# Kernel tuning notes

Measured on AMD Instinct MI355X. Metric: run time of the kernel, lower is better.

## Reference

```python
import jax, jax.numpy as jnp
import numpy as np
from jax.ops import segment_sum, segment_max

NUM_USERS = 100000
NUM_ITEMS = 50000
N_TOTAL = NUM_USERS + NUM_ITEMS
D = 64
E = 2000000
GCN_LAYERS = 3
GCN_LEFT = 0.5
GCN_RIGHT = 0.5
GCN_MEAN = True
USE_CL = True
CL_EPS = 0.2
CL_LAYER = 1
RF_LAYERS = 2
RF_TAU = 0.5
RF_ALPHA = 1.0


def setup_inputs() -> dict:
    key = jax.random.key(0)
    k1, k2, k3, k4, k5 = jax.random.split(key, 5)
    return {
        "user_emb": 0.1 * jax.random.normal(k1, (NUM_USERS, D), dtype=jnp.float32),
        "item_emb": 0.1 * jax.random.normal(k2, (NUM_ITEMS, D), dtype=jnp.float32),
        "noise": jax.random.uniform(k3, (GCN_LAYERS, N_TOTAL, D), dtype=jnp.float32),
        "edge_u": jax.random.randint(k4, (E,), 0, NUM_USERS, dtype=jnp.int32),
        "edge_i": jax.random.randint(k5, (E,), 0, NUM_ITEMS, dtype=jnp.int32),
    }


def _gcn_layer(emb, edge_u, edge_i, cu, ci):
    # LightGCN-style degree-normalized bipartite propagation over the edge list.
    ue, ie = emb[:NUM_USERS], emb[NUM_USERS:]
    # messages item -> user and user -> item, normalized by deg^-left * deg^-right
    msg_u = segment_sum(ie[edge_i] * (cu[edge_u] * ci[edge_i])[:, None], edge_u,
                        num_segments=NUM_USERS)
    msg_i = segment_sum(ue[edge_u] * (ci[edge_i] * cu[edge_u])[:, None], edge_i,
                        num_segments=NUM_ITEMS)
    return jnp.concatenate([msg_u, msg_i], axis=0)


def _rankformer_layer(emb, edge_u, edge_i):
    # Edge-sparse attention: per-edge score, segment softmax per node, weighted aggregate.
    ue, ie = emb[:NUM_USERS], emb[NUM_USERS:]
    eu_g, ei_g = ue[edge_u], ie[edge_i]            # [E, D] gathers
    s = RF_ALPHA * jnp.sum(eu_g * ei_g, axis=-1)   # [E]
    # user-side softmax over incident items
    mu = segment_max(s, edge_u, num_segments=NUM_USERS)
    pu = jnp.exp(s - mu[edge_u])
    zu = segment_sum(pu, edge_u, num_segments=NUM_USERS)
    rec_u = segment_sum(pu[:, None] * ei_g, edge_u, num_segments=NUM_USERS)
    rec_u = rec_u / jnp.maximum(zu, 1e-9)[:, None]
    # item-side softmax over incident users
    mi = segment_max(s, edge_i, num_segments=NUM_ITEMS)
    pi = jnp.exp(s - mi[edge_i])
    zi = segment_sum(pi, edge_i, num_segments=NUM_ITEMS)
    rec_i = segment_sum(pi[:, None] * eu_g, edge_i, num_segments=NUM_ITEMS)
    rec_i = rec_i / jnp.maximum(zi, 1e-9)[:, None]
    return jnp.concatenate([rec_u, rec_i], axis=0)


def reference(user_emb, item_emb, noise, edge_u, edge_i):
    ones = jnp.ones((E,), dtype=user_emb.dtype)
    du = jnp.maximum(segment_sum(ones, edge_u, num_segments=NUM_USERS), 1.0)
    di = jnp.maximum(segment_sum(ones, edge_i, num_segments=NUM_ITEMS), 1.0)
    cu = du ** (-GCN_LEFT)   # user-side normalization (left exponent)
    ci = di ** (-GCN_RIGHT)  # item-side normalization (right exponent)

    emb = jnp.concatenate([user_emb, item_emb], axis=0)  # [N_TOTAL, D]
    layer_embs = [emb]
    for layer in range(GCN_LAYERS):
        emb = _gcn_layer(emb, edge_u, edge_i, cu, ci)
        if USE_CL:
            nz = noise[layer]
            nz = nz / jnp.maximum(jnp.linalg.norm(nz, axis=-1, keepdims=True), 1e-12)
            emb = emb + jnp.sign(emb) * nz * CL_EPS
        layer_embs.append(emb)
    if GCN_MEAN:
        emb = jnp.mean(jnp.stack(layer_embs, axis=-1), axis=-1)

    for _ in range(RF_LAYERS):
        rec = _rankformer_layer(emb, edge_u, edge_i)
        emb = (1.0 - RF_TAU) * emb + RF_TAU * rec
    return emb
```

## Files before the change

### kernel.cpp

```cpp
#include <hip/hip_runtime.h>
#include <math.h>

#pragma clang fp contract(off)
#pragma clang fp reassociate(off)

#define NU 100000
#define NI 50000
#define NT 150000
#define DD 64
#define NE 2000000
#define NTD (NT * DD)
#define NPART 8
#define PARTW_U (NU / NPART)
#define PARTW_I (NI / NPART)
#define NCHUNK 256
#define CHW ((NE + NCHUNK - 1) / NCHUNK)

typedef _Float16 half4 __attribute__((ext_vector_type(4)));

__global__ __launch_bounds__(256) void count_ui_k(const int* __restrict__ eu, const int* __restrict__ ei,
                                                  int* __restrict__ cnt) {
  int part = blockIdx.x & 7;
  int side = (blockIdx.x >> 3) & 1;
  int chunk = blockIdx.x >> 4;
  int e0 = chunk * CHW;
  int e1 = e0 + CHW; if (e1 > NE) e1 = NE;
  if (side == 0) {
    int lo = part * PARTW_U, hi = lo + PARTW_U;
    for (int e = e0 + threadIdx.x; e < e1; e += 256) {
      int u = eu[e];
      if (u >= lo && u < hi) atomicAdd(&cnt[u], 1);
    }
  } else {
    int lo = part * PARTW_I, hi = lo + PARTW_I;
    for (int e = e0 + threadIdx.x; e < e1; e += 256) {
      int it = ei[e];
      if (it >= lo && it < hi) atomicAdd(&cnt[NU + it], 1);
    }
  }
}

__global__ __launch_bounds__(1024) void scanA_k(const int* __restrict__ cnt, int* __restrict__ lexcl,
                                                int* __restrict__ partials, int n) {
  int idx = blockIdx.x * 1024 + threadIdx.x;
  int v = (idx < n) ? cnt[idx] : 0;
  int lane = threadIdx.x & 63;
  int wid = threadIdx.x >> 6;
  int x = v;
#pragma unroll
  for (int off = 1; off < 64; off <<= 1) {
    int y = __shfl_up(x, off, 64);
    if (lane >= off) x += y;
  }
  __shared__ int wtot[16], woff[16];
  if (lane == 63) wtot[wid] = x;
  __syncthreads();
  if (threadIdx.x == 0) {
    int a = 0;
#pragma unroll
    for (int w = 0; w < 16; ++w) { woff[w] = a; a += wtot[w]; }
    partials[blockIdx.x] = a;
  }
  __syncthreads();
  if (idx < n) lexcl[idx] = x - v + woff[wid];
}

__global__ __launch_bounds__(64) void scanB_k(int* __restrict__ partials, int* __restrict__ row, int nchunks) {
  int lane = threadIdx.x;
  int carry = 0;
  for (int base = 0; base < nchunks; base += 64) {
    int idx = base + lane;
    int v = (idx < nchunks) ? partials[idx] : 0;
    int x = v;
#pragma unroll
    for (int off = 1; off < 64; off <<= 1) {
      int y = __shfl_up(x, off, 64);
      if (lane >= off) x += y;
    }
    if (idx < nchunks) partials[idx] = carry + x - v;
    carry += __shfl(x, 63, 64);
  }
  if (lane == 0) row[NT] = carry;
}

__global__ __launch_bounds__(1024) void scanC_k(int* __restrict__ row, int* __restrict__ cursor,
                                                float* __restrict__ coef, const int* __restrict__ partials, int n) {
  int idx = blockIdx.x * 1024 + threadIdx.x;
  if (idx >= n) return;
  int c = cursor[idx];
  int fin = row[idx] + partials[blockIdx.x];
  row[idx] = fin;
  cursor[idx] = fin;
  coef[idx] = (float)pow((double)(c > 0 ? c : 1), -0.5);
}

__global__ __launch_bounds__(256) void fill_ui_k(const int* __restrict__ eu, const int* __restrict__ ei,
                                                 int* __restrict__ cursor, int* __restrict__ eid) {
  int part = blockIdx.x & 7;
  int side = (blockIdx.x >> 3) & 1;
  int chunk = blockIdx.x >> 4;
  int e0 = chunk * CHW;
  int e1 = e0 + CHW; if (e1 > NE) e1 = NE;
  if (side == 0) {
    int lo = part * PARTW_U, hi = lo + PARTW_U;
    for (int e = e0 + threadIdx.x; e < e1; e += 256) {
      int u = eu[e];
      if (u >= lo && u < hi) {
        int p = atomicAdd(&cursor[u], 1);
        eid[p] = e;
      }
    }
  } else {
    int lo = part * PARTW_I, hi = lo + PARTW_I;
    for (int e = e0 + threadIdx.x; e < e1; e += 256) {
      int it = ei[e];
      if (it >= lo && it < hi) {
        int p = atomicAdd(&cursor[NU + it], 1);
        eid[p] = e;
      }
    }
  }
}

__global__ __launch_bounds__(256) void sort_k(const int* __restrict__ row, const int* __restrict__ eid,
                                              const int* __restrict__ eu, const int* __restrict__ ei,
                                              int* __restrict__ col) {
  int wv = (blockIdx.x * blockDim.x + threadIdx.x) >> 6;
  int lane = threadIdx.x & 63;
  if (wv >= NT) return;
  int beg = row[wv], end = row[wv + 1];
  for (int idx = beg + lane; idx < end; idx += 64) {
    int my = eid[idx];
    int r = 0;
    for (int j = beg; j < end; ++j) r += (eid[j] < my);
    col[beg + r] = (wv < NU) ? (NU + ei[my]) : eu[my];
  }
}

template <int FIRST, int LAST>
__global__ __launch_bounds__(256) void gcn4_k(const float* __restrict__ in, float* __restrict__ out,
                                              float* __restrict__ acc,
                                              const int* __restrict__ row, const int* __restrict__ col,
                                              const float* __restrict__ coef, const float* __restrict__ nz_l,
                                              const float* __restrict__ ue, const float* __restrict__ ie,
                                              _Float16* __restrict__ h16out) {
  int wave = (blockIdx.x * blockDim.x + threadIdx.x) >> 6;
  int lane = threadIdx.x & 63;
  int g = lane >> 4, q = lane & 15;
  int node = wave * 4 + g;
  if (node >= NT) return;
  int beg = row[node], end = row[node + 1];
  float cn = coef[node];
  float sx = 0.f, sy = 0.f, sz = 0.f, sw = 0.f;

  const float* gbase;
  if (FIRST) {
    gbase = (node < NU) ? (ie - (size_t)NU * DD) : ue;
  } else {
    gbase = in;
  }

#define GLD(dv, dc, kk) { int m_ = col[kk]; dc = coef[m_]; dv = *(const float4*)(gbase + (size_t)m_ * DD + q * 4); }
  float4 cv0, cv1, cv2, cv3;
  float cc0, cc1, cc2, cc3;
  int rem = end - beg;
  int k4end = end - (rem & 3);
  int k = beg;
  if (k < k4end) {
    GLD(cv0, cc0, k) GLD(cv1, cc1, k + 1) GLD(cv2, cc2, k + 2) GLD(cv3, cc3, k + 3)
  }
  for (; k < k4end; k += 4) {
    float4 nv0, nv1, nv2, nv3;
    float nc0, nc1, nc2, nc3;
    bool more = (k + 4) < k4end;
    if (more) {
      GLD(nv0, nc0, k + 4) GLD(nv1, nc1, k + 5) GLD(nv2, nc2, k + 6) GLD(nv3, nc3, k + 7)
    }
    {
      float w = cn * cc0;
      sx = sx + (cv0.x * w); sy = sy + (cv0.y * w); sz = sz + (cv0.z * w); sw = sw + (cv0.w * w);
    }
    {
      float w = cn * cc1;
      sx = sx + (cv1.x * w); sy = sy + (cv1.y * w); sz = sz + (cv1.z * w); sw = sw + (cv1.w * w);
    }
    {
      float w = cn * cc2;
      sx = sx + (cv2.x * w); sy = sy + (cv2.y * w); sz = sz + (cv2.z * w); sw = sw + (cv2.w * w);
    }
    {
      float w = cn * cc3;
      sx = sx + (cv3.x * w); sy = sy + (cv3.y * w); sz = sz + (cv3.z * w); sw = sw + (cv3.w * w);
    }
    if (more) {
      cv0 = nv0; cc0 = nc0; cv1 = nv1; cc1 = nc1;
      cv2 = nv2; cc2 = nc2; cv3 = nv3; cc3 = nc3;
    }
  }
  for (; k < end; ++k) {
    float4 v; float c;
    GLD(v, c, k)
    float w = cn * c;
    sx = sx + (v.x * w); sy = sy + (v.y * w); sz = sz + (v.z * w); sw = sw + (v.w * w);
  }
#undef GLD

  float4 nzv = *(const float4*)(nz_l + (size_t)node * DD + q * 4);
  float4 sq;
  sq.x = nzv.x * nzv.x; sq.y = nzv.y * nzv.y;
  sq.z = nzv.z * nzv.z; sq.w = nzv.w * nzv.w;
  float rA0 = 0.f, rA1 = 0.f, rA2 = 0.f, rA3 = 0.f;
  float rB0 = 0.f, rB1 = 0.f, rB2 = 0.f, rB3 = 0.f;
  int base = g * 16;
#pragma unroll
  for (int kk = 0; kk < 8; ++kk) {
    int le = base + 2 * kk, lo = le + 1;
    rA0 = rA0 + __shfl(sq.x, le, 64);
    rA1 = rA1 + __shfl(sq.y, le, 64);
    rA2 = rA2 + __shfl(sq.z, le, 64);
    rA3 = rA3 + __shfl(sq.w, le, 64);
    rB0 = rB0 + __shfl(sq.x, lo, 64);
    rB1 = rB1 + __shfl(sq.y, lo, 64);
    rB2 = rB2 + __shfl(sq.z, lo, 64);
    rB3 = rB3 + __shfl(sq.w, lo, 64);
  }
  float t01 = rA0 + rA1, t23 = rA2 + rA3;
  float t45 = rB0 + rB1, t67 = rB2 + rB3;
  float tot = (t01 + t23) + (t45 + t67);
  float nrm = __fsqrt_rn(tot);
  float den = fmaxf(nrm, 1e-12f);
  float4 o;
  {
    float nn = nzv.x / den;
    float sg = (sx > 0.f) ? 1.f : ((sx < 0.f) ? -1.f : 0.f);
    o.x = sx + ((sg * nn) * 0.2f);
  }
  {
    float nn = nzv.y / den;
    float sg = (sy > 0.f) ? 1.f : ((sy < 0.f) ? -1.f : 0.f);
    o.y = sy + ((sg * nn) * 0.2f);
  }
  {
    float nn = nzv.z / den;
    float sg = (sz > 0.f) ? 1.f : ((sz < 0.f) ? -1.f : 0.f);
    o.z = sz + ((sg * nn) * 0.2f);
  }
  {
    float nn = nzv.w / den;
    float sg = (sw > 0.f) ? 1.f : ((sw < 0.f) ? -1.f : 0.f);
    o.w = sw + ((sg * nn) * 0.2f);
  }
  size_t boff = (size_t)node * DD + q * 4;
  if (FIRST) {
    const float* ownp = (node < NU) ? (ue + (size_t)node * DD) : (ie + (size_t)(node - NU) * DD);
    float4 own = *(const float4*)(ownp + q * 4);
    *(float4*)(out + boff) = o;
    float4 a;
    a.x = own.x + o.x; a.y = own.y + o.y; a.z = own.z + o.z; a.w = own.w + o.w;
    *(float4*)(acc + boff) = a;
  } else {
    float4 a = *(const float4*)(acc + boff);
    if (LAST) {
      float4 mo;
      mo.x = (a.x + o.x) * 0.25f;
      mo.y = (a.y + o.y) * 0.25f;
      mo.z = (a.z + o.z) * 0.25f;
      mo.w = (a.w + o.w) * 0.25f;
      *(float4*)(out + boff) = mo;
      half4 hh;
      hh.x = (_Float16)mo.x; hh.y = (_Float16)mo.y;
      hh.z = (_Float16)mo.z; hh.w = (_Float16)mo.w;
      *(half4*)(h16out + boff) = hh;
    } else {
      *(float4*)(out + boff) = o;
      a.x = a.x + o.x; a.y = a.y + o.y; a.z = a.z + o.z; a.w = a.w + o.w;
      *(float4*)(acc + boff) = a;
    }
  }
}

template <int WRITEH>
__global__ __launch_bounds__(256) void rfaccum_k(const float* __restrict__ inF,
                                                 const _Float16* __restrict__ inH,
                                                 float* __restrict__ outF,
                                                 _Float16* __restrict__ outH,
                                                 const int* __restrict__ row, const int* __restrict__ col) {
  int wave = (blockIdx.x * blockDim.x + threadIdx.x) >> 6;
  int lane = threadIdx.x & 63;
  int g = lane >> 4, q = lane & 15;
  int node = wave * 4 + g;
  if (node >= NT) return;
  int beg = row[node], end = row[node + 1];
  size_t boff = (size_t)node * DD + q * 4;
  float4 e = *(const float4*)(inF + boff);
  float rx = 0.f, ry = 0.f, rz = 0.f, rw = 0.f, zacc = 0.f;

#define VLD(dv, kk) { dv = *(const half4*)(inH + (size_t)col[kk] * DD + q * 4); }
#define STEP(hv)                                                             \
  {                                                                          \
    float vx = (float)hv.x, vy = (float)hv.y, vz = (float)hv.z, vw = (float)hv.w; \
    float d = fmaf(e.x, vx, fmaf(e.y, vy, fmaf(e.z, vz, e.w * vw)));         \
    d += __shfl_xor(d, 1, 64); d += __shfl_xor(d, 2, 64);                    \
    d += __shfl_xor(d, 4, 64); d += __shfl_xor(d, 8, 64);                    \
    float p = __expf(d);                                                     \
    rx = fmaf(p, vx, rx); ry = fmaf(p, vy, ry);                              \
    rz = fmaf(p, vz, rz); rw = fmaf(p, vw, rw);                              \
    zacc = zacc + p;                                                         \
  }

  half4 cv0, cv1, cv2, cv3;
  int rem = end - beg;
  int k4end = end - (rem & 3);
  int k = beg;
  if (k < k4end) {
    VLD(cv0, k) VLD(cv1, k + 1) VLD(cv2, k + 2) VLD(cv3, k + 3)
  }
  for (; k < k4end; k += 4) {
    half4 nv0, nv1, nv2, nv3;
    bool more = (k + 4) < k4end;
    if (more) {
      VLD(nv0, k + 4) VLD(nv1, k + 5) VLD(nv2, k + 6) VLD(nv3, k + 7)
    }
    STEP(cv0) STEP(cv1) STEP(cv2) STEP(cv3)
    if (more) { cv0 = nv0; cv1 = nv1; cv2 = nv2; cv3 = nv3; }
  }
  for (; k < end; ++k) {
    half4 v;
    VLD(v, k)
    STEP(v)
  }
#undef STEP
#undef VLD

  float zi = 1.f / fmaxf(zacc, 1e-9f);
  float4 o;
  o.x = 0.5f * e.x + 0.5f * (rx * zi);
  o.y = 0.5f * e.y + 0.5f * (ry * zi);
  o.z = 0.5f * e.z + 0.5f * (rz * zi);
  o.w = 0.5f * e.w + 0.5f * (rw * zi);
  *(float4*)(outF + boff) = o;
  if (WRITEH) {
    half4 hh;
    hh.x = (_Float16)o.x; hh.y = (_Float16)o.y;
    hh.z = (_Float16)o.z; hh.w = (_Float16)o.w;
    *(half4*)(outH + boff) = hh;
  }
}

extern "C" void kernel_launch(void* const* d_in, const int* in_sizes, int n_in,
                              void* d_out, int out_size, void* d_ws, size_t ws_size,
                              hipStream_t stream) {
  const float* user_emb = (const float*)d_in[0];
  const float* item_emb = (const float*)d_in[1];
  const float* noise    = (const float*)d_in[2];
  const int*   edge_u   = (const int*)d_in[3];
  const int*   edge_i   = (const int*)d_in[4];
  float* out = (float*)d_out;

  float* embA = (float*)d_ws;
  float* embB = embA + (size_t)NTD;
  float* coef = embB + (size_t)NTD;
  int*   row  = (int*)(coef + (NT + 16));
  int*   cursor = row + (NT + 16);
  int*   partials = cursor + (NT + 16);
  int*   eidt = partials + 256;
  int*   col  = eidt + 2 * (size_t)NE;
  _Float16* H0 = (_Float16*)(col + 2 * (size_t)NE);
  _Float16* H1 = H0 + (size_t)NTD;

  float* acc = out;

  const int nchunks = (NT + 1023) / 1024;

  hipMemsetAsync(cursor, 0, (size_t)NT * sizeof(int), stream);
  count_ui_k<<<NCHUNK * NPART * 2, 256, 0, stream>>>(edge_u, edge_i, cursor);
  scanA_k<<<nchunks, 1024, 0, stream>>>(cursor, row, partials, NT);
  scanB_k<<<1, 64, 0, stream>>>(partials, row, nchunks);
  scanC_k<<<nchunks, 1024, 0, stream>>>(row, cursor, coef, partials, NT);
  fill_ui_k<<<NCHUNK * NPART * 2, 256, 0, stream>>>(edge_u, edge_i, cursor, eidt);

  const int gwave = (NT * 64 + 255) / 256;
  const int g4    = (NT / 4 * 64) / 256;

  sort_k<<<gwave, 256, 0, stream>>>(row, eidt, edge_u, edge_i, col);

  gcn4_k<1, 0><<<g4, 256, 0, stream>>>(nullptr, embB, acc, row, col, coef,
                                       noise + 0 * (size_t)NTD, user_emb, item_emb, nullptr);
  gcn4_k<0, 0><<<g4, 256, 0, stream>>>(embB, embA, acc, row, col, coef,
                                       noise + 1 * (size_t)NTD, user_emb, item_emb, nullptr);
  gcn4_k<0, 1><<<g4, 256, 0, stream>>>(embA, embB, acc, row, col, coef,
                                       noise + 2 * (size_t)NTD, user_emb, item_emb, H0);

  rfaccum_k<1><<<g4, 256, 0, stream>>>(embB, H0, embA, H1, row, col);
  rfaccum_k<0><<<g4, 256, 0, stream>>>(embA, H1, out, nullptr, row, col);
}
```

Baseline: 1.059 ms.

## Replace partitioned edge count/fill scans with a bucket pass plus per-bucket count/place

```diff
diff --git a/kernel.cpp b/kernel.cpp
--- a/kernel.cpp
+++ b/kernel.cpp
@@ -10,33 +10,65 @@
 #define DD 64
 #define NE 2000000
 #define NTD (NT * DD)
-#define NPART 8
-#define PARTW_U (NU / NPART)
-#define PARTW_I (NI / NPART)
-#define NCHUNK 256
-#define CHW ((NE + NCHUNK - 1) / NCHUNK)
+
+#define NBUCK 100
+#define BW_U 2000
+#define BW_I 1000
+#define NSUB 8
+#define SUBCAP 8192
 
 typedef _Float16 half4 __attribute__((ext_vector_type(4)));
 
-__global__ __launch_bounds__(256) void count_ui_k(const int* __restrict__ eu, const int* __restrict__ ei,
-                                                  int* __restrict__ cnt) {
-  int part = blockIdx.x & 7;
-  int side = (blockIdx.x >> 3) & 1;
-  int chunk = blockIdx.x >> 4;
-  int e0 = chunk * CHW;
-  int e1 = e0 + CHW; if (e1 > NE) e1 = NE;
-  if (side == 0) {
-    int lo = part * PARTW_U, hi = lo + PARTW_U;
-    for (int e = e0 + threadIdx.x; e < e1; e += 256) {
-      int u = eu[e];
-      if (u >= lo && u < hi) atomicAdd(&cnt[u], 1);
-    }
-  } else {
-    int lo = part * PARTW_I, hi = lo + PARTW_I;
-    for (int e = e0 + threadIdx.x; e < e1; e += 256) {
-      int it = ei[e];
-      if (it >= lo && it < hi) atomicAdd(&cnt[NU + it], 1);
-    }
+__global__ __launch_bounds__(256) void bucket_k(const int* __restrict__ eu, const int* __restrict__ ei,
+                                                int* __restrict__ bcur,
+                                                unsigned long long* __restrict__ bent) {
+  int c = blockIdx.x & 7;
+  int idx = blockIdx.x * 256 + threadIdx.x;
+  int stride = gridDim.x * 256;
+  for (int e = idx; e < NE; e += stride) {
+    int u = eu[e];
+    int b0 = u / BW_U;
+    int p0 = atomicAdd(&bcur[b0 * NSUB + c], 1);
+    if (p0 < SUBCAP)
+      bent[((size_t)(b0 * NSUB + c)) * SUBCAP + p0] =
+          ((unsigned long long)(unsigned)u << 32) | (unsigned)e;
+    int iv = ei[e];
+    int b1 = 50 + iv / BW_I;
+    int p1 = atomicAdd(&bcur[b1 * NSUB + c], 1);
+    if (p1 < SUBCAP)
+      bent[((size_t)(b1 * NSUB + c)) * SUBCAP + p1] =
+          ((unsigned long long)(unsigned)(NU + iv) << 32) | (unsigned)e;
+  }
+}
+
+__global__ __launch_bounds__(256) void bcount_k(const int* __restrict__ bcur,
+                                                const unsigned long long* __restrict__ bent,
+                                                int* __restrict__ cnt) {
+  int b = blockIdx.x % NBUCK;
+  int s = blockIdx.x / NBUCK;
+  int n = bcur[b * NSUB + s];
+  if (n > SUBCAP) n = SUBCAP;
+  const unsigned long long* src = bent + ((size_t)(b * NSUB + s)) * SUBCAP;
+  for (int j = threadIdx.x; j < n; j += 256) {
+    int dest = (int)(src[j] >> 32);
+    atomicAdd(&cnt[dest], 1);
+  }
+}
+
+__global__ __launch_bounds__(256) void place_k(const int* __restrict__ bcur,
+                                               const unsigned long long* __restrict__ bent,
+                                               int* __restrict__ cursor, int* __restrict__ eid) {
+  int b = blockIdx.x % NBUCK;
+  int s = blockIdx.x / NBUCK;
+  int n = bcur[b * NSUB + s];
+  if (n > SUBCAP) n = SUBCAP;
+  const unsigned long long* src = bent + ((size_t)(b * NSUB + s)) * SUBCAP;
+  for (int j = threadIdx.x; j < n; j += 256) {
+    unsigned long long v = src[j];
+    int dest = (int)(v >> 32);
+    int e = (int)(unsigned)v;
+    int p = atomicAdd(&cursor[dest], 1);
+    eid[p] = e;
   }
 }
 
@@ -92,34 +124,6 @@
   row[idx] = fin;
   cursor[idx] = fin;
   coef[idx] = (float)pow((double)(c > 0 ? c : 1), -0.5);
-}
-
-__global__ __launch_bounds__(256) void fill_ui_k(const int* __restrict__ eu, const int* __restrict__ ei,
-                                                 int* __restrict__ cursor, int* __restrict__ eid) {
-  int part = blockIdx.x & 7;
-  int side = (blockIdx.x >> 3) & 1;
-  int chunk = blockIdx.x >> 4;
-  int e0 = chunk * CHW;
-  int e1 = e0 + CHW; if (e1 > NE) e1 = NE;
-  if (side == 0) {
-    int lo = part * PARTW_U, hi = lo + PARTW_U;
-    for (int e = e0 + threadIdx.x; e < e1; e += 256) {
-      int u = eu[e];
-      if (u >= lo && u < hi) {
-        int p = atomicAdd(&cursor[u], 1);
-        eid[p] = e;
-      }
-    }
-  } else {
-    int lo = part * PARTW_I, hi = lo + PARTW_I;
-    for (int e = e0 + threadIdx.x; e < e1; e += 256) {
-      int it = ei[e];
-      if (it >= lo && it < hi) {
-        int p = atomicAdd(&cursor[NU + it], 1);
-        eid[p] = e;
-      }
-    }
-  }
 }
 
 __global__ __launch_bounds__(256) void sort_k(const int* __restrict__ row, const int* __restrict__ eid,
@@ -363,9 +367,11 @@
   int*   row  = (int*)(coef + (NT + 16));
   int*   cursor = row + (NT + 16);
   int*   partials = cursor + (NT + 16);
-  int*   eidt = partials + 256;
+  int*   bcur = partials + 256;
+  int*   eidt = bcur + 1024;
   int*   col  = eidt + 2 * (size_t)NE;
-  _Float16* H0 = (_Float16*)(col + 2 * (size_t)NE);
+  unsigned long long* bent = (unsigned long long*)(col + 2 * (size_t)NE);
+  _Float16* H0 = (_Float16*)bent;
   _Float16* H1 = H0 + (size_t)NTD;
 
   float* acc = out;
@@ -373,11 +379,14 @@
   const int nchunks = (NT + 1023) / 1024;
 
   hipMemsetAsync(cursor, 0, (size_t)NT * sizeof(int), stream);
-  count_ui_k<<<NCHUNK * NPART * 2, 256, 0, stream>>>(edge_u, edge_i, cursor);
+  hipMemsetAsync(bcur, 0, 1024 * sizeof(int), stream);
+
+  bucket_k<<<2048, 256, 0, stream>>>(edge_u, edge_i, bcur, bent);
+  bcount_k<<<NBUCK * NSUB, 256, 0, stream>>>(bcur, bent, cursor);
   scanA_k<<<nchunks, 1024, 0, stream>>>(cursor, row, partials, NT);
   scanB_k<<<1, 64, 0, stream>>>(partials, row, nchunks);
   scanC_k<<<nchunks, 1024, 0, stream>>>(row, cursor, coef, partials, NT);
-  fill_ui_k<<<NCHUNK * NPART * 2, 256, 0, stream>>>(edge_u, edge_i, cursor, eidt);
+  place_k<<<NBUCK * NSUB, 256, 0, stream>>>(bcur, bent, cursor, eidt);
 
   const int gwave = (NT * 64 + 255) / 256;
   const int g4    = (NT / 4 * 64) / 256;
```

Measured after the change: 2.497 ms. +135.7%, slower.
